# Kernel tuning notes

Hardware: AMD Instinct MI355X
Metric: run time of the kernel (lower is better)

## Reference

```python
import jax, jax.numpy as jnp
import numpy as np
import math

D_INPUT = 1024
D_Q = 1024
D_K = 1024
D_V = 1024
D_MODEL = 1024
B, S = 4, 2048


def setup_inputs() -> dict:
    key = jax.random.key(0)
    ks = jax.random.split(key, 9)
    sc = 0.02
    return {
        "x": jax.random.normal(ks[0], (B, S, D_INPUT), dtype=jnp.float32),
        "wq": jax.random.normal(ks[1], (D_INPUT, D_Q), dtype=jnp.float32) * sc,
        "bq": jnp.zeros((D_Q,), dtype=jnp.float32),
        "wk": jax.random.normal(ks[2], (D_INPUT, D_K), dtype=jnp.float32) * sc,
        "bk": jnp.zeros((D_K,), dtype=jnp.float32),
        "wv": jax.random.normal(ks[3], (D_INPUT, D_V), dtype=jnp.float32) * sc,
        "bv": jnp.zeros((D_V,), dtype=jnp.float32),
        "wp": jax.random.normal(ks[4], (D_V, D_MODEL), dtype=jnp.float32) * sc,
        "bp": jnp.zeros((D_MODEL,), dtype=jnp.float32),
    }


def reference(x, wq, bq, wk, bk, wv, bv, wp, bp):
    scale = math.sqrt(D_K)  # NOTE: original MULTIPLIES by sqrt(d_k)
    q = x @ wq + bq  # [B,S,Dq]
    k = x @ wk + bk  # [B,S,Dk]
    v = x @ wv + bv  # [B,S,Dv]
    scores = jnp.einsum('bsd,btd->bst', q, k) * scale
    p_attn = jax.nn.softmax(scores, axis=-1)
    # dropout: inference mode (training=False) -> identity
    context = jnp.einsum('bst,btd->bsd', p_attn, v)
    output = context @ wp + bp
    return (output, p_attn)
```

## Files before the change

### kernel.cpp

```cpp
#include <hip/hip_runtime.h>

typedef unsigned short u16;
typedef short bf16x8 __attribute__((ext_vector_type(8)));
typedef float floatx4 __attribute__((ext_vector_type(4)));

static __device__ __forceinline__ u16 f2bf(float f) {
  unsigned int u = __float_as_uint(f);
  unsigned int lsb = (u >> 16) & 1u;
  u += 0x7FFFu + lsb;
  return (u16)(u >> 16);
}
static __device__ __forceinline__ float bf2f(u16 u) {
  return __uint_as_float(((unsigned int)u) << 16);
}

static __device__ __forceinline__ void gl_lds16(const u16* g, u16* l) {
  __builtin_amdgcn_global_load_lds(
      (const __attribute__((address_space(1))) void*)g,
      (__attribute__((address_space(3))) void*)l, 16, 0, 0);
}

__global__ __launch_bounds__(256)
void prep_all(const float* __restrict__ wq, const float* __restrict__ wk,
              const float* __restrict__ wv, const float* __restrict__ wp,
              const float* __restrict__ bq, const float* __restrict__ bk,
              const float* __restrict__ x,
              u16* __restrict__ qkThi, u16* __restrict__ qkTlo,
              u16* __restrict__ wvThi, u16* __restrict__ wpThi,
              float* __restrict__ bqk,
              u16* __restrict__ xhi, u16* __restrict__ xlo,
              u16* __restrict__ xThi) {
  __shared__ float t[32][33];
  const int z = blockIdx.z;
  const int tid = threadIdx.x;
  const int lr = tid >> 3;
  const int lc = (tid & 7) * 4;

  if (z == 4) {
    if (blockIdx.y == 0 && blockIdx.x < 8) {
      const int i = blockIdx.x * 256 + tid;
      bqk[i] = (i < 1024) ? bq[i] : bk[i - 1024];
    }
    return;
  }

  if (z >= 5) {
    const int r0 = ((z - 5) * 32 + blockIdx.y) * 32;
    const int c0 = blockIdx.x * 32;
    float4 v = *(const float4*)(x + (size_t)(r0 + lr) * 1024 + c0 + lc);
    float f[4] = {v.x, v.y, v.z, v.w};
    t[lr][lc + 0] = v.x; t[lr][lc + 1] = v.y; t[lr][lc + 2] = v.z; t[lr][lc + 3] = v.w;
    u16 ph[4], pl[4];
#pragma unroll
    for (int j = 0; j < 4; j++) {
      ph[j] = f2bf(f[j]);
      pl[j] = f2bf(f[j] - bf2f(ph[j]));
    }
    const size_t o = (size_t)(r0 + lr) * 1024 + c0 + lc;
    *(uint2*)(xhi + o) = *(uint2*)ph;
    *(uint2*)(xlo + o) = *(uint2*)pl;
    __syncthreads();
    u16 pt[4];
#pragma unroll
    for (int j = 0; j < 4; j++) pt[j] = f2bf(t[lc + j][lr]);
    const int b = r0 >> 11, rt = r0 & 2047;
    *(uint2*)(xThi + (size_t)b * (1024 * 2048) + (size_t)(c0 + lr) * 2048 + rt + lc) =
        *(uint2*)pt;
    return;
  }

  const float* in = (z == 0) ? wq : (z == 1) ? wk : (z == 2) ? wv : wp;
  u16* hi = (z == 2) ? wvThi : (z == 3) ? wpThi : (qkThi + (size_t)z * 1024 * 1024);
  u16* lo = (z == 0) ? qkTlo : (z == 1) ? (qkTlo + 1024 * 1024) : (u16*)nullptr;
  const int want_lo = (z < 2);

  const int r0 = blockIdx.y * 32, c0 = blockIdx.x * 32;
  float4 v = *(const float4*)(in + (size_t)(r0 + lr) * 1024 + c0 + lc);
  t[lr][lc + 0] = v.x; t[lr][lc + 1] = v.y; t[lr][lc + 2] = v.z; t[lr][lc + 3] = v.w;
  __syncthreads();
  u16 ph[4], pl[4];
#pragma unroll
  for (int j = 0; j < 4; j++) {
    float f = t[lc + j][lr];
    ph[j] = f2bf(f);
    if (want_lo) pl[j] = f2bf(f - bf2f(ph[j]));
  }
  const size_t o = (size_t)(c0 + lr) * 1024 + r0 + lc;
  *(uint2*)(hi + o) = *(uint2*)ph;
  if (want_lo) *(uint2*)(lo + o) = *(uint2*)pl;
}

template<int KB, int ASP, int BSP, int OM, int HB>
__global__ __launch_bounds__(256)
void gemm_mfma(const u16* __restrict__ Ahi, const u16* __restrict__ Alo,
               const u16* __restrict__ Bhi, const u16* __restrict__ Blo,
               const float* __restrict__ bias,
               void* __restrict__ C0, void* __restrict__ C1,
               void* __restrict__ C2, void* __restrict__ C3,
               int N, int K, int lda, int ldb, int ldc,
               long long aB, long long bB, long long cB, float scale) {
  constexpr int CM = KB / 8 - 1;
  constexpr int RPI = 512 / KB;
  constexpr int NI = KB / 16;
  constexpr int PL = 128 * KB;
  __shared__ __align__(16) u16 As[(1 + ASP) * PL];
  __shared__ __align__(16) u16 Bs[(1 + BSP) * PL];

  const int bz = blockIdx.z;
  const u16* A0 = Ahi + (size_t)bz * aB;
  const u16* A1 = ASP ? (Alo + (size_t)bz * aB) : (const u16*)nullptr;
  const u16* B0 = Bhi + (size_t)bz * bB;
  const u16* B1 = BSP ? (Blo + (size_t)bz * bB) : (const u16*)nullptr;

  const int m0 = blockIdx.y * 128;
  const int n0 = blockIdx.x * 128;
  const int tid = threadIdx.x;
  const int w = tid >> 6;
  const int L = tid & 63;
  const int rr = L & 15, quad = L >> 4;
  const int wm = (w >> 1) * 64, wn = (w & 1) * 64;

  const int lrow = (KB == 32) ? (L >> 2) : (L >> 3);
  const int c3 = (L & CM) ^ ((L >> 3) & CM);
  const int srow = w * 32 + lrow;
  u16* stA = &As[w * 32 * KB];
  u16* stB = &Bs[w * 32 * KB];
  const u16* gA0 = A0 + (size_t)(m0 + srow) * lda + c3 * 8;
  const u16* gA1 = ASP ? A1 + (size_t)(m0 + srow) * lda + c3 * 8 : (const u16*)nullptr;
  const u16* gB0 = B0 + (size_t)(n0 + srow) * ldb + c3 * 8;
  const u16* gB1 = BSP ? B1 + (size_t)(n0 + srow) * ldb + c3 * 8 : (const u16*)nullptr;

  floatx4 acc[4][4] = {};

  for (int k0 = 0; k0 < K; k0 += KB) {
#pragma unroll
    for (int q = 0; q < NI; q++) {
      gl_lds16(gA0 + k0 + (size_t)q * RPI * lda, stA + q * 512);
      gl_lds16(gB0 + k0 + (size_t)q * RPI * ldb, stB + q * 512);
    }
    if (ASP) {
#pragma unroll
      for (int q = 0; q < NI; q++)
        gl_lds16(gA1 + k0 + (size_t)q * RPI * lda, stA + PL + q * 512);
    }
    if (BSP) {
#pragma unroll
      for (int q = 0; q < NI; q++)
        gl_lds16(gB1 + k0 + (size_t)q * RPI * ldb, stB + PL + q * 512);
    }
    __syncthreads();

#pragma unroll
    for (int s = 0; s < KB / 32; s++) {
      const int pcb = ((KB == 32) ? (quad ^ ((rr >> 1) & 3))
                                  : ((s * 4 + quad) ^ (rr & 7))) * 8;
      bf16x8 a0[4], a1[4], b0[4], b1[4];
#pragma unroll
      for (int i = 0; i < 4; i++) {
        const int arow = wm + i * 16 + rr;
        const int brow = wn + i * 16 + rr;
        a0[i] = *(const bf16x8*)&As[arow * KB + pcb];
        b0[i] = *(const bf16x8*)&Bs[brow * KB + pcb];
        if (ASP) a1[i] = *(const bf16x8*)&As[PL + arow * KB + pcb];
        if (BSP) b1[i] = *(const bf16x8*)&Bs[PL + brow * KB + pcb];
      }
#pragma unroll
      for (int i = 0; i < 4; i++) {
#pragma unroll
        for (int j = 0; j < 4; j++) {
          acc[i][j] = __builtin_amdgcn_mfma_f32_16x16x32_bf16(a0[i], b0[j], acc[i][j], 0, 0, 0);
          if (ASP && BSP) {
            acc[i][j] = __builtin_amdgcn_mfma_f32_16x16x32_bf16(a0[i], b1[j], acc[i][j], 0, 0, 0);
            acc[i][j] = __builtin_amdgcn_mfma_f32_16x16x32_bf16(a1[i], b0[j], acc[i][j], 0, 0, 0);
          }
        }
      }
    }
    __syncthreads();
  }

#pragma unroll
  for (int i = 0; i < 4; i++) {
    const int mbase = m0 + wm + i * 16 + quad * 4;
#pragma unroll
    for (int j = 0; j < 4; j++) {
      const int col = n0 + wn + j * 16 + rr;
      float bvs = 0.f;
      if (HB) bvs = bias[col];
      if (OM == 5) {
        u16* hi; u16* lo;
        if (col < 1024) { hi = (u16*)C0; lo = (u16*)C1; }
        else            { hi = (u16*)C2; lo = (u16*)C3; }
        const int cc = col & 1023;
#pragma unroll
        for (int ii = 0; ii < 4; ii++) {
          const float v = acc[i][j][ii] + bvs;
          const size_t idx = (size_t)(mbase + ii) * 1024 + cc;
          const u16 h = f2bf(v);
          hi[idx] = h;
          lo[idx] = f2bf(v - bf2f(h));
        }
      } else {
        u16* Cb = (u16*)C0 + (size_t)bz * cB;
        float* Cf = (float*)C0 + (size_t)bz * cB;
        u16* Cl = (OM == 1) ? ((u16*)C1 + (size_t)bz * cB) : (u16*)nullptr;
#pragma unroll
        for (int ii = 0; ii < 4; ii++) {
          const float v = acc[i][j][ii] * scale + bvs;
          const size_t idx = (size_t)(mbase + ii) * ldc + col;
          if (OM == 0) {
            Cb[idx] = f2bf(v);
          } else if (OM == 1) {
            const u16 h = f2bf(v);
            Cb[idx] = h;
            Cl[idx] = f2bf(v - bf2f(h));
          } else {
            Cf[idx] = v;
          }
        }
      }
    }
  }
}

__global__ __launch_bounds__(256)
void softmax_rows(float* __restrict__ S, u16* __restrict__ Pb) {
  const int row = blockIdx.x;
  float* s = S + (size_t)row * 2048;
  const int tid = threadIdx.x;
  const int w = tid >> 6;
  __shared__ float redm[4];
  __shared__ float reds[4];

  float v[8];
  float mx = -1e30f;
#pragma unroll
  for (int i = 0; i < 8; i++) {
    v[i] = s[tid + 256 * i];
    mx = fmaxf(mx, v[i]);
  }
#pragma unroll
  for (int o = 32; o > 0; o >>= 1) mx = fmaxf(mx, __shfl_xor(mx, o, 64));
  if ((tid & 63) == 0) redm[w] = mx;
  __syncthreads();
  mx = fmaxf(fmaxf(redm[0], redm[1]), fmaxf(redm[2], redm[3]));

  float sum = 0.f;
#pragma unroll
  for (int i = 0; i < 8; i++) {
    v[i] = __expf(v[i] - mx);
    sum += v[i];
  }
#pragma unroll
  for (int o = 32; o > 0; o >>= 1) sum += __shfl_xor(sum, o, 64);
  if ((tid & 63) == 0) reds[w] = sum;
  __syncthreads();
  sum = reds[0] + reds[1] + reds[2] + reds[3];
  const float rs = 1.0f / sum;
#pragma unroll
  for (int i = 0; i < 8; i++) {
    const float p = v[i] * rs;
    s[tid + 256 * i] = p;
    Pb[(size_t)row * 2048 + tid + 256 * i] = f2bf(p);
  }
}

extern "C" void kernel_launch(void* const* d_in, const int* in_sizes, int n_in,
                              void* d_out, int out_size, void* d_ws, size_t ws_size,
                              hipStream_t stream) {
  const float* x  = (const float*)d_in[0];
  const float* wq = (const float*)d_in[1];
  const float* bq = (const float*)d_in[2];
  const float* wk = (const float*)d_in[3];
  const float* bk = (const float*)d_in[4];
  const float* wv = (const float*)d_in[5];
  const float* bv = (const float*)d_in[6];
  const float* wp = (const float*)d_in[7];
  const float* bp = (const float*)d_in[8];

  const size_t MB = 1024 * 1024;
  char* ws = (char*)d_ws;
  u16* qkThi = (u16*)(ws + 0 * MB);
  u16* qkTlo = (u16*)(ws + 4 * MB);
  u16* wvThi = (u16*)(ws + 8 * MB);
  u16* wpThi = (u16*)(ws + 10 * MB);
  float* bqk = (float*)(ws + 12 * MB);
  u16* xhi   = (u16*)(ws + 13 * MB);
  u16* xlo   = (u16*)(ws + 29 * MB);
  u16* qhi   = (u16*)(ws + 45 * MB);
  u16* qlo   = (u16*)(ws + 61 * MB);
  u16* khi   = (u16*)(ws + 77 * MB);
  u16* klo   = (u16*)(ws + 93 * MB);
  u16* xThi  = (u16*)(ws + 109 * MB);
  u16* pbf   = khi;
  u16* px    = qhi;
  u16* ctx   = qlo;

  float* outp = (float*)d_out;
  float* scf  = (float*)d_out + 8388608;

  const dim3 blk(256);

  prep_all<<<dim3(32, 32, 13), blk, 0, stream>>>(
      wq, wk, wv, wp, bq, bk, x, qkThi, qkTlo, wvThi, wpThi, bqk, xhi, xlo, xThi);

  gemm_mfma<32, 1, 1, 5, 1><<<dim3(16, 64, 1), blk, 0, stream>>>(
      xhi, xlo, qkThi, qkTlo, bqk, qhi, qlo, khi, klo,
      2048, 1024, 1024, 1024, 1024, 0, 0, 0, 1.0f);

  gemm_mfma<32, 1, 1, 2, 0><<<dim3(16, 16, 4), blk, 0, stream>>>(
      qhi, qlo, khi, klo, nullptr, scf, nullptr, nullptr, nullptr,
      2048, 1024, 1024, 1024, 2048,
      2048LL * 1024, 2048LL * 1024, 2048LL * 2048, 32.0f);

  softmax_rows<<<dim3(8192), blk, 0, stream>>>(scf, pbf);

  gemm_mfma<64, 0, 0, 0, 0><<<dim3(8, 16, 4), blk, 0, stream>>>(
      pbf, nullptr, xThi, nullptr, nullptr, px, nullptr, nullptr, nullptr,
      1024, 2048, 2048, 2048, 1024,
      2048LL * 2048, 1024LL * 2048, 2048LL * 1024, 1.0f);

  gemm_mfma<64, 0, 0, 0, 1><<<dim3(8, 64, 1), blk, 0, stream>>>(
      px, nullptr, wvThi, nullptr, bv, ctx, nullptr, nullptr, nullptr,
      1024, 1024, 1024, 1024, 1024, 0, 0, 0, 1.0f);

  gemm_mfma<64, 0, 0, 2, 1><<<dim3(8, 64, 1), blk, 0, stream>>>(
      ctx, nullptr, wpThi, nullptr, bp, outp, nullptr, nullptr, nullptr,
      1024, 1024, 1024, 1024, 1024, 0, 0, 0, 1.0f);
}
```

Measured before the change: 479.5 us.

## Add 256x256 8-wave pipelined split-bf16 GEMM kernel for QK projection and scores

Adds a specialized gemm8 kernel that uses 512 threads and 256x256 output tiles. It runs a 4-stage global_load_lds ring buffer with explicit vmcnt waits, barrier-interleaved MFMA halves, setprio, and an XCD-aware block remap. It handles the hi/lo split-bf16 products (hi*hi, hi*lo, lo*hi) as a single 96-half-step K loop. It replaces the two generic gemm_mfma launches for the fused QK projection and the score computation, aiming for more data reuse per tile and better overlap of loads with compute. The trade-offs are hardcoded dimensions, 128KB of LDS per block, and fewer blocks in the grid.

```diff
diff --git a/kernel.cpp b/kernel.cpp
--- a/kernel.cpp
+++ b/kernel.cpp
@@ -218,6 +218,149 @@
             Cf[idx] = v;
           }
         }
+      }
+    }
+  }
+}
+
+template<int OM>
+__global__ __launch_bounds__(512, 2)
+void gemm8(const u16* __restrict__ Ahi, const u16* __restrict__ Alo,
+           const u16* __restrict__ Bhi, const u16* __restrict__ Blo,
+           const float* __restrict__ bias,
+           void* __restrict__ C0, void* __restrict__ C1,
+           void* __restrict__ C2, void* __restrict__ C3,
+           long long aB, long long bB, long long cB, float scale) {
+  __shared__ __align__(16) u16 As[4 * 8192];
+  __shared__ __align__(16) u16 Bs[4 * 8192];
+
+  const int gx = gridDim.x, gy = gridDim.y, gz = gridDim.z;
+  const int flat = blockIdx.x + gx * (blockIdx.y + gy * blockIdx.z);
+  const int nwg = gx * gy * gz;
+  const int lg = (flat & 7) * (nwg >> 3) + (flat >> 3);
+  const int bx = lg % gx;
+  const int by = (lg / gx) % gy;
+  const int bz = lg / (gx * gy);
+
+  const int m0 = by * 256, n0 = bx * 256;
+  const u16* pAhi = Ahi + (size_t)bz * aB;
+  const u16* pAlo = Alo + (size_t)bz * aB;
+  const u16* pBhi = Bhi + (size_t)bz * bB;
+  const u16* pBlo = Blo + (size_t)bz * bB;
+
+  const int tid = threadIdx.x;
+  const int w = tid >> 6;
+  const int L = tid & 63;
+  const int rr = L & 15, quad = L >> 4;
+  const int wm = (w >> 2) * 128;
+  const int wn = (w & 3) * 64;
+
+  const int rbase = w * 16 + (L >> 2);
+  const int coff = (((L & 3) ^ ((L >> 2) & 3)) << 3);
+  const int arow = (m0 + rbase) * 1024 + coff;
+  const int brow = (n0 + rbase) * 1024 + coff;
+  u16* const ldA = As + w * 512;
+  u16* const ldB = Bs + w * 512;
+
+  const int aoff = ((wm + rr) << 5) + ((quad ^ (rr & 3)) << 3);
+  const int boff = ((wn + rr) << 5) + ((quad ^ (rr & 3)) << 3);
+
+  auto stageA = [&](int H) {
+    const int kt = H >> 1;
+    const u16* src = (kt < 32) ? pAhi : pAlo;
+    const int koff = ((kt & 15) << 6) + ((H & 1) << 5);
+    const u16* g = src + arow + koff;
+    u16* l = ldA + (H & 3) * 8192;
+    gl_lds16(g, l);
+    gl_lds16(g + 128 * 1024, l + 4096);
+  };
+  auto stageB = [&](int H) {
+    const int kt = H >> 1;
+    const u16* src = (kt < 16) ? pBhi : (kt < 32) ? pBlo : pBhi;
+    const int koff = ((kt & 15) << 6) + ((H & 1) << 5);
+    const u16* g = src + brow + koff;
+    u16* l = ldB + (H & 3) * 8192;
+    gl_lds16(g, l);
+    gl_lds16(g + 128 * 1024, l + 4096);
+  };
+
+  floatx4 acc[8][4] = {};
+
+#define PAIR(H, SB2, SA3, VM)                                                  \
+  {                                                                            \
+    __builtin_amdgcn_sched_barrier(0);                                         \
+    const u16* ab = As + ((H) & 3) * 8192 + aoff;                              \
+    const u16* bb = Bs + ((H) & 3) * 8192 + boff;                              \
+    bf16x8 a[8], b0, b1, b2, b3;                                               \
+    _Pragma("unroll")                                                          \
+    for (int i = 0; i < 8; i++) a[i] = *(const bf16x8*)(ab + i * 512);         \
+    b0 = *(const bf16x8*)(bb);                                                 \
+    b1 = *(const bf16x8*)(bb + 512);                                           \
+    if (SB2) stageB((H) + 2);                                                  \
+    __builtin_amdgcn_s_barrier();                                              \
+    asm volatile("s_waitcnt lgkmcnt(0)");                                      \
+    __builtin_amdgcn_s_setprio(1);                                             \
+    _Pragma("unroll")                                                          \
+    for (int i = 0; i < 8; i++) {                                              \
+      acc[i][0] = __builtin_amdgcn_mfma_f32_16x16x32_bf16(a[i], b0, acc[i][0], 0, 0, 0); \
+      acc[i][1] = __builtin_amdgcn_mfma_f32_16x16x32_bf16(a[i], b1, acc[i][1], 0, 0, 0); \
+    }                                                                          \
+    __builtin_amdgcn_s_setprio(0);                                             \
+    __builtin_amdgcn_s_barrier();                                              \
+    b2 = *(const bf16x8*)(bb + 1024);                                          \
+    b3 = *(const bf16x8*)(bb + 1536);                                          \
+    if (SA3) stageA((H) + 3);                                                  \
+    __builtin_amdgcn_s_barrier();                                              \
+    asm volatile("s_waitcnt lgkmcnt(0)");                                      \
+    __builtin_amdgcn_s_setprio(1);                                             \
+    _Pragma("unroll")                                                          \
+    for (int i = 0; i < 8; i++) {                                              \
+      acc[i][2] = __builtin_amdgcn_mfma_f32_16x16x32_bf16(a[i], b2, acc[i][2], 0, 0, 0); \
+      acc[i][3] = __builtin_amdgcn_mfma_f32_16x16x32_bf16(a[i], b3, acc[i][3], 0, 0, 0); \
+    }                                                                          \
+    __builtin_amdgcn_s_setprio(0);                                             \
+    if ((VM) == 6) asm volatile("s_waitcnt vmcnt(6)");                         \
+    else if ((VM) == 4) asm volatile("s_waitcnt vmcnt(4)");                    \
+    else if ((VM) == 0) asm volatile("s_waitcnt vmcnt(0)");                    \
+    __builtin_amdgcn_s_barrier();                                              \
+  }
+
+  stageA(0); stageB(0); stageA(1); stageB(1); stageA(2);
+  asm volatile("s_waitcnt vmcnt(6)");
+  __builtin_amdgcn_s_barrier();
+
+  for (int H = 0; H <= 92; ++H)
+    PAIR(H, true, true, 6);
+  PAIR(93, true, false, 4);
+  PAIR(94, false, false, 0);
+  PAIR(95, false, false, -1);
+#undef PAIR
+
+#pragma unroll
+  for (int i = 0; i < 8; i++) {
+    const int mb = m0 + wm + i * 16 + quad * 4;
+#pragma unroll
+    for (int j = 0; j < 4; j++) {
+      const int col = n0 + wn + j * 16 + rr;
+      if (OM == 5) {
+        u16* hi; u16* lo;
+        if (col < 1024) { hi = (u16*)C0; lo = (u16*)C1; }
+        else            { hi = (u16*)C2; lo = (u16*)C3; }
+        const int cc = col & 1023;
+        const float bvs = bias[col];
+#pragma unroll
+        for (int ii = 0; ii < 4; ii++) {
+          const float v = acc[i][j][ii] + bvs;
+          const size_t idx = (size_t)(mb + ii) * 1024 + cc;
+          const u16 h = f2bf(v);
+          hi[idx] = h;
+          lo[idx] = f2bf(v - bf2f(h));
+        }
+      } else {
+        float* Cf = (float*)C0 + (size_t)bz * cB;
+#pragma unroll
+        for (int ii = 0; ii < 4; ii++)
+          Cf[(size_t)(mb + ii) * 2048 + col] = acc[i][j][ii] * scale;
       }
     }
   }
@@ -304,13 +447,11 @@
   prep_all<<<dim3(32, 32, 13), blk, 0, stream>>>(
       wq, wk, wv, wp, bq, bk, x, qkThi, qkTlo, wvThi, wpThi, bqk, xhi, xlo, xThi);
 
-  gemm_mfma<32, 1, 1, 5, 1><<<dim3(16, 64, 1), blk, 0, stream>>>(
-      xhi, xlo, qkThi, qkTlo, bqk, qhi, qlo, khi, klo,
-      2048, 1024, 1024, 1024, 1024, 0, 0, 0, 1.0f);
-
-  gemm_mfma<32, 1, 1, 2, 0><<<dim3(16, 16, 4), blk, 0, stream>>>(
+  gemm8<5><<<dim3(8, 32, 1), dim3(512), 0, stream>>>(
+      xhi, xlo, qkThi, qkTlo, bqk, qhi, qlo, khi, klo, 0, 0, 0, 1.0f);
+
+  gemm8<2><<<dim3(8, 8, 4), dim3(512), 0, stream>>>(
       qhi, qlo, khi, klo, nullptr, scf, nullptr, nullptr, nullptr,
-      2048, 1024, 1024, 1024, 2048,
       2048LL * 1024, 2048LL * 1024, 2048LL * 2048, 32.0f);
 
   softmax_rows<<<dim3(8192), blk, 0, stream>>>(scf, pbf);
```

Result: slower. 521.0 us (+8.7%).
